# Performance work log

Measured on AMD Instinct MI355X. Metric: run time of the kernel, lower is better.

## Reference

```python
import jax, jax.numpy as jnp
import numpy as np

WIN_LEN = 400
WIN_INC = 100
FFT_LEN = 512
EPSILON = float(np.finfo(np.float32).eps)


def _make_kernel():
    # periodic (fftbins=True) hamming window, matching scipy.signal.get_window
    n = np.arange(WIN_LEN)
    window = 0.54 - 0.46 * np.cos(2.0 * np.pi * n / WIN_LEN)
    # direct-DFT basis: rfft of identity, truncated to win_len taps
    fourier_basis = np.fft.rfft(np.eye(FFT_LEN))[:WIN_LEN]          # [win_len, fft_len//2+1]
    kernel = np.concatenate([fourier_basis.real, fourier_basis.imag], axis=1).T  # [2*(fft//2+1), win_len]
    kernel = kernel * window                                        # window applied per tap
    return kernel[:, None, :].astype(np.float32)                    # [514, 1, 400] (OIH)


def setup_inputs() -> dict:
    key = jax.random.key(0)
    inputs = jax.random.normal(key, (16, 160000), dtype=jnp.float32)  # [B, L] waveform
    weight = jnp.asarray(_make_kernel())                              # fixed DFT buffer
    return {"inputs": inputs, "weight": weight}


def reference(inputs, weight):
    pad = WIN_LEN - WIN_INC  # 300
    x = inputs[:, None, :]                                   # [B, 1, L]
    x = jnp.pad(x, ((0, 0), (0, 0), (pad, pad)))             # symmetric pad, as in F.pad
    out = jax.lax.conv_general_dilated(
        x, weight,
        window_strides=(WIN_INC,),
        padding='VALID',
        dimension_numbers=('NCH', 'OIH', 'NCH'),
    )                                                        # [B, 514, T]
    r, i = jnp.split(out, 2, axis=1)                         # real / imag halves [B, 257, T]
    mags = jnp.sqrt(jnp.clip(r * r + i * i, EPSILON))
    phase = jnp.arctan2(i + EPSILON, r + EPSILON)
    return mags, phase
```

## Files before the change

kernel.cpp:

```cpp
#include <hip/hip_runtime.h>
#include <math.h>


#define BATCH 16
#define NSAMP 160000
#define NF 257
#define NT 1603
#define KLEN 400
#define INC 100
#define PADL 300
#define EPSF 1.1920928955078125e-7f
#define TAU 1e-2f

#define FPB 16
#define ZSTR 258
#define XSPAN ((FPB - 1) * INC + KLEN)
#define NTB ((NT + FPB - 1) / FPB)

__global__ __launch_bounds__(256, 3)
void stft_fft(const float* __restrict__ x, const float* __restrict__ w,
              float* __restrict__ out) {
  __shared__ float2 Z[FPB * ZSTR];
  __shared__ float2 tw[256];
  __shared__ float y256[FPB];
  __shared__ __align__(16) float xs[XSPAN];
  __shared__ __align__(16) float win[KLEN];

  const int tid = threadIdx.x;
  const int t0 = blockIdx.x * FPB;
  const int b = blockIdx.y;
  const int tl = tid & 15;
  const int th = tid >> 4;

  const long xb = (long)b * NSAMP;
  const int base = t0 * INC - PADL;
  for (int r = 0; r < 2; ++r) {
    int i4 = r * 256 + tid;
    if (4 * i4 < XSPAN) {
      int g = base + 4 * i4;
      float4 v;
      if (g >= 0 && g + 3 < NSAMP) {
        v = *(const float4*)(x + xb + g);
      } else {
        v.x = (g + 0 >= 0 && g + 0 < NSAMP) ? x[xb + g + 0] : 0.f;
        v.y = (g + 1 >= 0 && g + 1 < NSAMP) ? x[xb + g + 1] : 0.f;
        v.z = (g + 2 >= 0 && g + 2 < NSAMP) ? x[xb + g + 2] : 0.f;
        v.w = (g + 3 >= 0 && g + 3 < NSAMP) ? x[xb + g + 3] : 0.f;
      }
      *(float4*)&xs[4 * i4] = v;
    }
  }
  if (tid < KLEN / 4) {
    *(float4*)&win[4 * tid] = *(const float4*)(w + 4 * tid);
  }
  {
    double a = (double)tid * (6.283185307179586476925286766559 / 512.0);
    tw[tid] = make_float2((float)cos(a), (float)(-sin(a)));
  }
  __syncthreads();

  for (int r = 0; r < 16; ++r) {
    int m = r * 16 + th;
    float2 zv = make_float2(0.f, 0.f);
    if (m < 200) {
      float2 xv = *(const float2*)&xs[tl * INC + 2 * m];
      float2 wv = *(const float2*)&win[2 * m];
      zv = make_float2(xv.x * wv.x, xv.y * wv.y);
    }
    int p = __brev((unsigned)m) >> 24;
    Z[tl * ZSTR + p] = zv;
  }

  for (int s = 0; s < 8; ++s) {
    __syncthreads();
    const int half = 1 << s;
    for (int r = 0; r < 8; ++r) {
      int j = r * 16 + th;
      int q = j & (half - 1);
      int i0 = ((j >> s) << (s + 1)) | q;
      float2* Zt = Z + tl * ZSTR;
      float2 a = Zt[i0];
      float2 bb = Zt[i0 + half];
      float2 wv = tw[q << (8 - s)];
      float2 bt = make_float2(bb.x * wv.x - bb.y * wv.y,
                              bb.x * wv.y + bb.y * wv.x);
      Zt[i0] = make_float2(a.x + bt.x, a.y + bt.y);
      Zt[i0 + half] = make_float2(a.x - bt.x, a.y - bt.y);
    }
  }
  __syncthreads();

  for (int r = 0; r < 9; ++r) {
    int tau = r * 256 + tid;
    if (tau < FPB * 129) {
      int t = tau & 15;
      int p = tau >> 4;
      float2* Zt = Z + t * ZSTR;
      float2 z0 = Zt[p];
      float2 z1 = Zt[(256 - p) & 255];
      float2 ze = make_float2(0.5f * (z0.x + z1.x), 0.5f * (z0.y - z1.y));
      float2 zo = make_float2(0.5f * (z0.y + z1.y), 0.5f * (z1.x - z0.x));
      float2 T = tw[p];
      float2 tz = make_float2(zo.x * T.x - zo.y * T.y,
                              zo.x * T.y + zo.y * T.x);
      Zt[p] = make_float2(ze.x + tz.x, ze.y + tz.y);
      float2 yb = make_float2(ze.x - tz.x, tz.y - ze.y);
      if (p == 0) y256[t] = yb.x;
      else Zt[256 - p] = yb;
    }
  }
  __syncthreads();

  const long plane = (long)BATCH * NF * NT;
  const long pb = (long)b * NF * NT;
  for (int r = 0; r < 17; ++r) {
    int tau = r * 256 + tid;
    if (tau < NF * FPB) {
      int t = tau & 15;
      int ff = tau >> 4;
      int tt = t0 + t;
      if (tt < NT) {
        float rr, ii;
        if (ff < 256) {
          float2 v = Z[t * ZSTR + ff];
          rr = v.x; ii = v.y;
        } else {
          rr = y256[t]; ii = 0.f;
        }
        float ie = ii + EPSF, re = rr + EPSF;
        if (fabsf(ie) < TAU && re < TAU) {
          const float* wr = w + (long)ff * KLEN;
          const float* wi = w + (long)(257 + ff) * KLEN;
          const float* xf = &xs[t * INC];
          float r2 = 0.f, i2 = 0.f;
          for (int k = 0; k < KLEN; ++k) {
            float xv = xf[k];
            r2 = fmaf(wr[k], xv, r2);
            i2 = fmaf(wi[k], xv, i2);
          }
          rr = r2; ii = i2;
        }
        long o = pb + (long)ff * NT + tt;
        out[o] = sqrtf(fmaxf(rr * rr + ii * ii, EPSF));
        out[o + plane] = atan2f(ii + EPSF, rr + EPSF);
      }
    }
  }
}

extern "C" void kernel_launch(void* const* d_in, const int* in_sizes, int n_in,
                              void* d_out, int out_size, void* d_ws, size_t ws_size,
                              hipStream_t stream) {
  const float* x = (const float*)d_in[0];
  const float* w = (const float*)d_in[1];
  float* out = (float*)d_out;

  dim3 grid(NTB, BATCH);
  stft_fft<<<grid, dim3(256), 0, stream>>>(x, w, out);
}
```

Baseline: 176.4 us.

## Replace radix-2 shared-memory FFT with register 16x16 four-step FFT and fuse output

Replaces the 8-stage radix-2 butterfly loop, which needed a barrier per stage and round-trips through shared memory, with a four-step 16x16 decomposition. Each thread runs 16-point DIF FFTs in registers, with one twiddle pass and a transpose through shared memory in between. The real-FFT post-processing now writes magnitude and phase directly instead of storing back to shared memory, which removes another barrier and the separate output loop. The cost is higher register pressure from the float2[16] arrays, plus a more divergent emit path, since each thread now handles two bins.

```diff
diff --git a/kernel.cpp b/kernel.cpp
--- a/kernel.cpp
+++ b/kernel.cpp
@@ -17,12 +17,82 @@
 #define XSPAN ((FPB - 1) * INC + KLEN)
 #define NTB ((NT + FPB - 1) / FPB)
 
+__device__ __forceinline__ float2 cmul(float2 a, float2 b) {
+  return make_float2(a.x * b.x - a.y * b.y, a.x * b.y + a.y * b.x);
+}
+
+__device__ __forceinline__ void fft16_dif(float2* a) {
+  const float C1 = 0.92387953251128674f;
+  const float S1 = 0.38268343236508978f;
+  const float R2 = 0.70710678118654752f;
+  {
+    const float2 W[8] = {{1.f, 0.f},  {C1, -S1},  {R2, -R2},  {S1, -C1},
+                         {0.f, -1.f}, {-S1, -C1}, {-R2, -R2}, {-C1, -S1}};
+    #pragma unroll
+    for (int j = 0; j < 8; ++j) {
+      float2 u = a[j], v = a[j + 8];
+      a[j] = make_float2(u.x + v.x, u.y + v.y);
+      float2 d = make_float2(u.x - v.x, u.y - v.y);
+      a[j + 8] = cmul(d, W[j]);
+    }
+  }
+  {
+    const float2 W[4] = {{1.f, 0.f}, {R2, -R2}, {0.f, -1.f}, {-R2, -R2}};
+    #pragma unroll
+    for (int h = 0; h < 16; h += 8)
+      #pragma unroll
+      for (int j = 0; j < 4; ++j) {
+        float2 u = a[h + j], v = a[h + j + 4];
+        a[h + j] = make_float2(u.x + v.x, u.y + v.y);
+        float2 d = make_float2(u.x - v.x, u.y - v.y);
+        a[h + j + 4] = cmul(d, W[j]);
+      }
+  }
+  #pragma unroll
+  for (int q = 0; q < 16; q += 4) {
+    float2 u0 = a[q], v0 = a[q + 2];
+    a[q] = make_float2(u0.x + v0.x, u0.y + v0.y);
+    a[q + 2] = make_float2(u0.x - v0.x, u0.y - v0.y);
+    float2 u1 = a[q + 1], v1 = a[q + 3];
+    a[q + 1] = make_float2(u1.x + v1.x, u1.y + v1.y);
+    float2 d = make_float2(u1.x - v1.x, u1.y - v1.y);
+    a[q + 3] = make_float2(d.y, -d.x);
+  }
+  #pragma unroll
+  for (int q = 0; q < 16; q += 2) {
+    float2 u = a[q], v = a[q + 1];
+    a[q] = make_float2(u.x + v.x, u.y + v.y);
+    a[q + 1] = make_float2(u.x - v.x, u.y - v.y);
+  }
+}
+
+__device__ __forceinline__ void emit_fp(float rr, float ii, int ff,
+                                        const float* __restrict__ w,
+                                        const float* xf,
+                                        float* __restrict__ out,
+                                        long o, long plane) {
+  float ie = ii + EPSF, re = rr + EPSF;
+  if (fabsf(ie) < TAU && re < TAU) {
+    const float* wr = w + (long)ff * KLEN;
+    const float* wi = w + (long)(257 + ff) * KLEN;
+    float r2 = 0.f, i2 = 0.f;
+    for (int k = 0; k < KLEN; ++k) {
+      float xv = xf[k];
+      r2 = fmaf(wr[k], xv, r2);
+      i2 = fmaf(wi[k], xv, i2);
+    }
+    rr = r2; ii = i2;
+  }
+  out[o] = sqrtf(fmaxf(rr * rr + ii * ii, EPSF));
+  out[o + plane] = atan2f(ii + EPSF, rr + EPSF);
+}
+
 __global__ __launch_bounds__(256, 3)
-void stft_fft(const float* __restrict__ x, const float* __restrict__ w,
-              float* __restrict__ out) {
+void stft_fft4(const float* __restrict__ x, const float* __restrict__ w,
+               float* __restrict__ out) {
   __shared__ float2 Z[FPB * ZSTR];
-  __shared__ float2 tw[256];
-  __shared__ float y256[FPB];
+  __shared__ float2 tw[132];
+  __shared__ float2 tw256[256];
   __shared__ __align__(16) float xs[XSPAN];
   __shared__ __align__(16) float win[KLEN];
 
@@ -54,42 +124,62 @@
     *(float4*)&win[4 * tid] = *(const float4*)(w + 4 * tid);
   }
   {
+    double a = (double)tid * (6.283185307179586476925286766559 / 256.0);
+    tw256[tid] = make_float2((float)cos(a), (float)(-sin(a)));
+  }
+  if (tid < 132) {
     double a = (double)tid * (6.283185307179586476925286766559 / 512.0);
     tw[tid] = make_float2((float)cos(a), (float)(-sin(a)));
   }
   __syncthreads();
 
+  float2 a[16];
+  const float* xf = &xs[tl * INC];
+  #pragma unroll
+  for (int n1 = 0; n1 < 12; ++n1) {
+    int n = 32 * n1 + 2 * th;
+    float2 xv = *(const float2*)&xf[n];
+    float2 wv = *(const float2*)&win[n];
+    a[n1] = make_float2(xv.x * wv.x, xv.y * wv.y);
+  }
+  {
+    int n = 384 + 2 * th;
+    if (n < KLEN) {
+      float2 xv = *(const float2*)&xf[n];
+      float2 wv = *(const float2*)&win[n];
+      a[12] = make_float2(xv.x * wv.x, xv.y * wv.y);
+    } else {
+      a[12] = make_float2(0.f, 0.f);
+    }
+  }
+  a[13] = a[14] = a[15] = make_float2(0.f, 0.f);
+
+  fft16_dif(a);
+
+  static const int BR[16] = {0, 8, 4, 12, 2, 10, 6, 14,
+                             1, 9, 5, 13, 3, 11, 7, 15};
+  float2* Zf = Z + tl * ZSTR;
+  #pragma unroll
   for (int r = 0; r < 16; ++r) {
-    int m = r * 16 + th;
-    float2 zv = make_float2(0.f, 0.f);
-    if (m < 200) {
-      float2 xv = *(const float2*)&xs[tl * INC + 2 * m];
-      float2 wv = *(const float2*)&win[2 * m];
-      zv = make_float2(xv.x * wv.x, xv.y * wv.y);
-    }
-    int p = __brev((unsigned)m) >> 24;
-    Z[tl * ZSTR + p] = zv;
-  }
-
-  for (int s = 0; s < 8; ++s) {
-    __syncthreads();
-    const int half = 1 << s;
-    for (int r = 0; r < 8; ++r) {
-      int j = r * 16 + th;
-      int q = j & (half - 1);
-      int i0 = ((j >> s) << (s + 1)) | q;
-      float2* Zt = Z + tl * ZSTR;
-      float2 a = Zt[i0];
-      float2 bb = Zt[i0 + half];
-      float2 wv = tw[q << (8 - s)];
-      float2 bt = make_float2(bb.x * wv.x - bb.y * wv.y,
-                              bb.x * wv.y + bb.y * wv.x);
-      Zt[i0] = make_float2(a.x + bt.x, a.y + bt.y);
-      Zt[i0 + half] = make_float2(a.x - bt.x, a.y - bt.y);
-    }
+    const int k1 = BR[r];
+    float2 v = (k1 == 0) ? a[r] : cmul(a[r], tw256[th * k1]);
+    Zf[th * 16 + k1] = v;
   }
   __syncthreads();
 
+  float2 g[16];
+  #pragma unroll
+  for (int n2 = 0; n2 < 16; ++n2) g[n2] = Zf[n2 * 16 + th];
+  fft16_dif(g);
+  #pragma unroll
+  for (int r = 0; r < 16; ++r) {
+    const int k2 = BR[r];
+    Zf[16 * k2 + th] = g[r];
+  }
+  __syncthreads();
+
+  const long plane = (long)BATCH * NF * NT;
+  const long pb = (long)b * NF * NT;
   for (int r = 0; r < 9; ++r) {
     int tau = r * 256 + tid;
     if (tau < FPB * 129) {
@@ -101,48 +191,19 @@
       float2 ze = make_float2(0.5f * (z0.x + z1.x), 0.5f * (z0.y - z1.y));
       float2 zo = make_float2(0.5f * (z0.y + z1.y), 0.5f * (z1.x - z0.x));
       float2 T = tw[p];
-      float2 tz = make_float2(zo.x * T.x - zo.y * T.y,
-                              zo.x * T.y + zo.y * T.x);
-      Zt[p] = make_float2(ze.x + tz.x, ze.y + tz.y);
+      float2 tz = cmul(zo, T);
+      float2 ya = make_float2(ze.x + tz.x, ze.y + tz.y);
       float2 yb = make_float2(ze.x - tz.x, tz.y - ze.y);
-      if (p == 0) y256[t] = yb.x;
-      else Zt[256 - p] = yb;
-    }
-  }
-  __syncthreads();
-
-  const long plane = (long)BATCH * NF * NT;
-  const long pb = (long)b * NF * NT;
-  for (int r = 0; r < 17; ++r) {
-    int tau = r * 256 + tid;
-    if (tau < NF * FPB) {
-      int t = tau & 15;
-      int ff = tau >> 4;
       int tt = t0 + t;
       if (tt < NT) {
-        float rr, ii;
-        if (ff < 256) {
-          float2 v = Z[t * ZSTR + ff];
-          rr = v.x; ii = v.y;
+        const float* xfr = &xs[t * INC];
+        emit_fp(ya.x, ya.y, p, w, xfr, out, pb + (long)p * NT + tt, plane);
+        if (p == 0) {
+          emit_fp(yb.x, 0.f, 256, w, xfr, out, pb + (long)256 * NT + tt, plane);
         } else {
-          rr = y256[t]; ii = 0.f;
+          emit_fp(yb.x, yb.y, 256 - p, w, xfr, out,
+                  pb + (long)(256 - p) * NT + tt, plane);
         }
-        float ie = ii + EPSF, re = rr + EPSF;
-        if (fabsf(ie) < TAU && re < TAU) {
-          const float* wr = w + (long)ff * KLEN;
-          const float* wi = w + (long)(257 + ff) * KLEN;
-          const float* xf = &xs[t * INC];
-          float r2 = 0.f, i2 = 0.f;
-          for (int k = 0; k < KLEN; ++k) {
-            float xv = xf[k];
-            r2 = fmaf(wr[k], xv, r2);
-            i2 = fmaf(wi[k], xv, i2);
-          }
-          rr = r2; ii = i2;
-        }
-        long o = pb + (long)ff * NT + tt;
-        out[o] = sqrtf(fmaxf(rr * rr + ii * ii, EPSF));
-        out[o + plane] = atan2f(ii + EPSF, rr + EPSF);
       }
     }
   }
@@ -156,5 +217,5 @@
   float* out = (float*)d_out;
 
   dim3 grid(NTB, BATCH);
-  stft_fft<<<grid, dim3(256), 0, stream>>>(x, w, out);
-}
+  stft_fft4<<<grid, dim3(256), 0, stream>>>(x, w, out);
+}
```

Measured after the change: 156.0 us. 11.5% less time.
